# Optimization experiments

Measured on AMD Instinct MI355X. Metric: run time of the kernel, lower is better.

Reference implementation:

```python
import jax, jax.numpy as jnp
from jax import lax
import numpy as np

N, E, L, H, B, R = 12800, 204800, 24, 128, 64, 8
VN, VA = 100, 20


def _p(key, *shape):
    return jax.random.normal(key, shape, dtype=jnp.float32) * 0.05


def setup_inputs() -> dict:
    key = jax.random.key(0)
    ks = jax.random.split(key, 32)
    inp = {
        'nodeTypes': jax.random.randint(ks[0], (N,), 0, VN),
        'edge_index': jax.random.randint(ks[1], (2, E), 0, N),
        'edge_attr': jax.random.randint(ks[2], (E,), 0, R),
        'bs': jnp.repeat(jnp.arange(B, dtype=jnp.int32), N // B),
        'sequence_input': jax.random.uniform(ks[3], (N, L), dtype=jnp.float32),
        'nodes_bs': jnp.full((B,), N // B, dtype=jnp.int32),
        'len_seq': jnp.full((B,), L, dtype=jnp.int32),
        'action_input': jax.random.randint(ks[4], (B,), 0, VA),
        # parameters (RGCN weights SHARED across the 2 layers, as in the source)
        'emb_nodes_w': _p(ks[5], VN, H),
        'emb_actions_w': _p(ks[6], VA, H),
        'rgcn_W': _p(ks[7], R, H, H),
        'rgcn_root': _p(ks[8], H, H),
        'rgcn_b': _p(ks[9], H),
        'gru_Wih': _p(ks[10], 3 * H, H),
        'gru_Whh': _p(ks[11], 3 * H, H),
        'gru_bih': _p(ks[12], 3 * H),
        'gru_bhh': _p(ks[13], 3 * H),
        'linA_w': _p(ks[14], H, H),
        'linA_b': _p(ks[15], H),
        'linAf_w': _p(ks[16], VA, H),
        'linAf_b': _p(ks[17], VA),
        'linN_w': _p(ks[18], H, 2 * H),
        'linN_b': _p(ks[19], H),
        'linNf_w': _p(ks[20], 1, H),
        'linNf_b': _p(ks[21], 1),
        'fin_w': _p(ks[22], H, H),
        'fin_b': _p(ks[23], H),
        'finf_w': _p(ks[24], 1, H),
        'finf_b': _p(ks[25], 1),
    }
    return inp


def _rgcn(x, src, dst, etype, W, Wroot, b):
    # PyG RGCNConv: per-relation mean aggregation, then per-relation weight, plus root + bias
    comb = dst * R + etype  # combined (node, relation) segment id
    msg = jax.ops.segment_sum(x[src], comb, num_segments=N * R)  # [N*R, H]
    cnt = jax.ops.segment_sum(jnp.ones((src.shape[0],), x.dtype), comb, num_segments=N * R)
    mean = (msg / jnp.maximum(cnt, 1.0)[:, None]).reshape(N, R, H)
    return jnp.einsum('nrh,rhd->nd', mean, W) + x @ Wroot + b


def _gru(x_seq, h0, Wih, Whh, bih, bhh):
    # torch GRU gate order: r, z, n ; x_seq [B, T, H]
    def step(h, x):
        gi = x @ Wih.T + bih
        gh = h @ Whh.T + bhh
        i_r, i_z, i_n = jnp.split(gi, 3, axis=-1)
        h_r, h_z, h_n = jnp.split(gh, 3, axis=-1)
        r = jax.nn.sigmoid(i_r + h_r)
        z = jax.nn.sigmoid(i_z + h_z)
        n = jnp.tanh(i_n + r * h_n)
        h_new = (1.0 - z) * n + z * h
        return h_new, h_new
    _, ys = lax.scan(step, h0, jnp.swapaxes(x_seq, 0, 1))
    return jnp.swapaxes(ys, 0, 1)


def _seg_softmax(x, seg, nseg):
    m = jax.ops.segment_max(x, seg, num_segments=nseg)
    e = jnp.exp(x - m[seg])
    s = jax.ops.segment_sum(e, seg, num_segments=nseg)
    return e / s[seg]


def reference(nodeTypes, edge_index, edge_attr, bs, sequence_input, nodes_bs, len_seq,
              action_input, emb_nodes_w, emb_actions_w, rgcn_W, rgcn_root, rgcn_b,
              gru_Wih, gru_Whh, gru_bih, gru_bhh, linA_w, linA_b, linAf_w, linAf_b,
              linN_w, linN_b, linNf_w, linNf_b, fin_w, fin_b, finf_w, finf_b):
    src, dst = edge_index[0], edge_index[1]
    x = emb_nodes_w[nodeTypes]
    for _ in range(2):  # shared-weight RGCN layers + ReLU
        x = jax.nn.relu(_rgcn(x, src, dst, edge_attr, rgcn_W, rgcn_root, rgcn_b))
    nodeEmb = x  # [N, H]

    cnt = jax.ops.segment_sum(jnp.ones((N,), x.dtype), bs, num_segments=B)
    h_G = jax.ops.segment_sum(nodeEmb, bs, num_segments=B) / cnt[:, None]  # [B, H]

    action = jax.nn.relu(h_G @ linA_w.T + linA_b) @ linAf_w.T + linAf_b  # [B, VA]
    final = jax.nn.sigmoid(jax.nn.relu(h_G @ fin_w.T + fin_b) @ finf_w.T + finf_b)  # [B, 1]

    sos = emb_actions_w[action_input][:, None, :]  # [B, 1, H]
    # scatter-sum of per-timestep weighted node embeddings -> [B, L, H]
    emb_seq = sequence_input[:, :, None] * nodeEmb[:, None, :]  # [N, L, H]
    agg = jax.ops.segment_sum(emb_seq, bs, num_segments=B)
    input_gru = jnp.concatenate([sos, agg], axis=1)[:, :L]  # len_seq == L drops last step
    seq = _gru(input_gru, h_G, gru_Wih, gru_Whh, gru_bih, gru_bhh)  # [B, L, H]

    # linNodes(cat(out_gru, nodeEmb)) computed without materializing the [N,L,2H] concat
    part1 = jnp.einsum('blh,oh->blo', seq, linN_w[:, :H])[bs]      # [N, L, H]
    part2 = nodeEmb @ linN_w[:, H:].T                               # [N, H]
    hidden = jax.nn.relu(part1 + part2[:, None, :] + linN_b)       # [N, L, H]
    logits = jnp.einsum('nlh,h->nl', hidden, linNf_w[0]) + linNf_b[0]  # [N, L]
    nodes_final = _seg_softmax(logits, bs, B)
    return (action, nodes_final, final)
```

## Files before the change

kernel.cpp:

```cpp
#include <hip/hip_runtime.h>
#include <math.h>

#define NN 12800
#define NE 204800
#define LL 24
#define HH 128
#define BB 64
#define RR 8
#define VAx 20
#define KC 1152
#define CHK 8
#define PS 16

typedef __attribute__((ext_vector_type(8))) short bf16x8;
typedef __attribute__((ext_vector_type(4))) float f32x4;

__device__ inline unsigned short f2bf(float f) {
  unsigned u = __float_as_uint(f);
  unsigned r = u + 0x7FFF + ((u >> 16) & 1);
  return (unsigned short)(r >> 16);
}
__device__ inline float bf2f(unsigned short s) {
  return __uint_as_float(((unsigned)s) << 16);
}
__device__ inline unsigned packbf(float lo, float hi) {
  return (unsigned)f2bf(lo) | ((unsigned)f2bf(hi) << 16);
}

__global__ void k_prep(const float* __restrict__ rgcnW, const float* __restrict__ rgcnRoot,
                       unsigned short* __restrict__ wcatT,
                       const float* __restrict__ linN_w, unsigned short* __restrict__ linN2bt,
                       const float* __restrict__ Wih, unsigned short* __restrict__ Wihbt,
                       const float* __restrict__ Whh, float* __restrict__ WhhT,
                       const float* __restrict__ linA_w, float* __restrict__ linAT,
                       const float* __restrict__ fin_w, float* __restrict__ finT,
                       unsigned short* __restrict__ linN1bt,
                       const int* __restrict__ nt, const float* __restrict__ embN,
                       unsigned int* __restrict__ x, int* __restrict__ deg) {
  int idx = blockIdx.x * 256 + threadIdx.x;
  if (idx < HH * KC) {
    int d = idx / KC, k = idx - d * KC;
    float v = (k < 1024) ? rgcnW[(k >> 7) * (HH * HH) + (k & 127) * HH + d]
                         : rgcnRoot[(k - 1024) * HH + d];
    wcatT[idx] = f2bf(v);
    return;
  }
  idx -= HH * KC;
  if (idx < HH * HH) {
    int d = idx >> 7, k = idx & 127;
    linN2bt[idx] = f2bf(linN_w[d * 2 * HH + HH + k]);
    return;
  }
  idx -= HH * HH;
  if (idx < 3 * HH * HH) {
    Wihbt[idx] = f2bf(Wih[idx]);
    return;
  }
  idx -= 3 * HH * HH;
  if (idx < 3 * HH * HH) {
    int r = idx / HH, c = idx - r * HH;
    WhhT[c * 384 + r] = Whh[r * HH + c];
    return;
  }
  idx -= 3 * HH * HH;
  if (idx < HH * HH) {
    int r = idx >> 7, c = idx & 127;
    linAT[c * HH + r] = linA_w[r * HH + c];
    return;
  }
  idx -= HH * HH;
  if (idx < HH * HH) {
    int r = idx >> 7, c = idx & 127;
    finT[c * HH + r] = fin_w[r * HH + c];
    return;
  }
  idx -= HH * HH;
  if (idx < HH * HH) {
    int o = idx >> 7, k = idx & 127;
    linN1bt[idx] = f2bf(linN_w[o * 2 * HH + k]);
    return;
  }
  idx -= HH * HH;
  if (idx < NN * 64) {
    int n = idx >> 6, p = idx & 63;
    const float* e = embN + (size_t)nt[n] * HH + p * 2;
    x[idx] = packbf(e[0], e[1]);
    return;
  }
  idx -= NN * 64;
  if (idx < NN * PS) deg[idx] = 0;
}
#define PREP_TOTAL (HH * KC + HH * HH + 3 * HH * HH + 3 * HH * HH + HH * HH + HH * HH + HH * HH + NN * 64 + NN * PS)

__global__ void k_count(const int* __restrict__ edst, int* __restrict__ deg,
                        const int* __restrict__ bs, int* __restrict__ bptr) {
  int i = blockIdx.x * 256 + threadIdx.x;
  if (i < NE) atomicAdd(&deg[edst[i] * PS], 1);
  if (i < NN) {
    int b = bs[i];
    if (i == 0 || bs[i - 1] != b) bptr[b] = i;
    if (i == NN - 1) bptr[BB] = NN;
  }
}

__global__ __launch_bounds__(1024) void k_scane(const int* __restrict__ deg,
                                                int* __restrict__ indptr,
                                                int* __restrict__ cur) {
  __shared__ int ws[16];
  int tid = threadIdx.x;
  const int per = (NN + 1023) >> 10;
  int i0 = tid * per;
  int s = 0;
  for (int k = 0; k < per; ++k) {
    int i = i0 + k;
    if (i < NN) s += deg[i * PS];
  }
  int lane = tid & 63, wv = tid >> 6;
  int incl = s;
#pragma unroll
  for (int off = 1; off < 64; off <<= 1) {
    int t = __shfl_up(incl, off);
    if (lane >= off) incl += t;
  }
  if (lane == 63) ws[wv] = incl;
  __syncthreads();
  if (tid < 16) {
    int v = ws[tid];
    int inc = v;
#pragma unroll
    for (int off = 1; off < 16; off <<= 1) {
      int t = __shfl_up(inc, off);
      if (tid >= off) inc += t;
    }
    ws[tid] = inc - v;
  }
  __syncthreads();
  int run = ws[wv] + incl - s;
  for (int k = 0; k < per; ++k) {
    int i = i0 + k;
    if (i < NN) {
      indptr[i] = run;
      cur[i * PS] = run;
      run += deg[i * PS];
      if (i == NN - 1) indptr[NN] = run;
    }
  }
}

__global__ void k_scattere(const int* __restrict__ esrc, const int* __restrict__ edst,
                           const int* __restrict__ erel, int* __restrict__ cur,
                           int* __restrict__ esort) {
  int i = blockIdx.x * 256 + threadIdx.x;
  if (i >= NE) return;
  int p = atomicAdd(&cur[edst[i] * PS], 1);
  esort[p] = esrc[i] | (erel[i] << 16);
}

__global__ __launch_bounds__(256) void k_agg(const unsigned int* __restrict__ x,
                                             const int* __restrict__ indptr,
                                             const int* __restrict__ esort,
                                             unsigned int* __restrict__ A, int n0, int nc) {
  int wid = ((blockIdx.x * 256) + threadIdx.x) >> 6;
  int lane = threadIdx.x & 63;
  if (wid >= nc) return;
  int n = n0 + wid;
  float a0=0,a1=0,a2=0,a3=0,a4=0,a5=0,a6=0,a7=0;
  float b0=0,b1=0,b2=0,b3=0,b4=0,b5=0,b6=0,b7=0;
  int c0=0,c1=0,c2=0,c3=0,c4=0,c5=0,c6=0,c7=0;
  int e0 = indptr[n], e1 = indptr[n + 1];

#define ACCV(RV, VV)                                                              \
  {                                                                               \
    float v0_ = bf2f((unsigned short)((VV) & 0xFFFF));                            \
    float v1_ = bf2f((unsigned short)((VV) >> 16));                               \
    switch (RV) {                                                                 \
      case 0: a0 += v0_; b0 += v1_; c0++; break;                                  \
      case 1: a1 += v0_; b1 += v1_; c1++; break;                                  \
      case 2: a2 += v0_; b2 += v1_; c2++; break;                                  \
      case 3: a3 += v0_; b3 += v1_; c3++; break;                                  \
      case 4: a4 += v0_; b4 += v1_; c4++; break;                                  \
      case 5: a5 += v0_; b5 += v1_; c5++; break;                                  \
      case 6: a6 += v0_; b6 += v1_; c6++; break;                                  \
      default: a7 += v0_; b7 += v1_; c7++; break;                                 \
    }                                                                             \
  }

  int e = e0;
  for (; e + 4 <= e1; e += 4) {
    int pk0 = esort[e], pk1 = esort[e + 1], pk2 = esort[e + 2], pk3 = esort[e + 3];
    unsigned v0 = x[(size_t)(pk0 & 0xFFFF) * 64 + lane];
    unsigned v1 = x[(size_t)(pk1 & 0xFFFF) * 64 + lane];
    unsigned v2 = x[(size_t)(pk2 & 0xFFFF) * 64 + lane];
    unsigned v3 = x[(size_t)(pk3 & 0xFFFF) * 64 + lane];
    ACCV(pk0 >> 16, v0);
    ACCV(pk1 >> 16, v1);
    ACCV(pk2 >> 16, v2);
    ACCV(pk3 >> 16, v3);
  }
  for (; e < e1; ++e) {
    int pk = esort[e];
    unsigned v = x[(size_t)(pk & 0xFFFF) * 64 + lane];
    ACCV(pk >> 16, v);
  }
#undef ACCV

  unsigned int* Ar = A + (size_t)wid * (KC / 2);
  float i0 = 1.0f / (float)(c0 > 0 ? c0 : 1);
  float i1 = 1.0f / (float)(c1 > 0 ? c1 : 1);
  float i2 = 1.0f / (float)(c2 > 0 ? c2 : 1);
  float i3 = 1.0f / (float)(c3 > 0 ? c3 : 1);
  float i4 = 1.0f / (float)(c4 > 0 ? c4 : 1);
  float i5 = 1.0f / (float)(c5 > 0 ? c5 : 1);
  float i6 = 1.0f / (float)(c6 > 0 ? c6 : 1);
  float i7 = 1.0f / (float)(c7 > 0 ? c7 : 1);
  Ar[0 * 64 + lane] = packbf(a0 * i0, b0 * i0);
  Ar[1 * 64 + lane] = packbf(a1 * i1, b1 * i1);
  Ar[2 * 64 + lane] = packbf(a2 * i2, b2 * i2);
  Ar[3 * 64 + lane] = packbf(a3 * i3, b3 * i3);
  Ar[4 * 64 + lane] = packbf(a4 * i4, b4 * i4);
  Ar[5 * 64 + lane] = packbf(a5 * i5, b5 * i5);
  Ar[6 * 64 + lane] = packbf(a6 * i6, b6 * i6);
  Ar[7 * 64 + lane] = packbf(a7 * i7, b7 * i7);
  Ar[512 + lane] = x[n * 64 + lane];
}

template <int OUTMODE>
__global__ __launch_bounds__(256) void k_mgemm(const unsigned short* __restrict__ Abf, int lda,
                                               const unsigned short* __restrict__ BTbf, int ldb,
                                               const float* __restrict__ bias,
                                               void* __restrict__ C, int ldc, int M, int K) {
  __shared__ unsigned int ldsu[(8192 + 16384) / 4];
  char* ldsc = (char*)ldsu;
  int tid = threadIdx.x;
  int m0 = blockIdx.x * 64;
  int n0c = blockIdx.y * 128;
  int w = tid >> 6, l = tid & 63;
  int lrow = l & 15, lg = l >> 4;
  f32x4 acc[8] = {};

  const char* Ab = (const char*)Abf;
  const char* Bb = (const char*)(BTbf + (size_t)n0c * ldb);
  int KT = K >> 6;
  for (int kt = 0; kt < KT; ++kt) {
    int k0 = kt << 6;
#pragma unroll
    for (int i = 0; i < 2; ++i) {
      int slot = i * 256 + tid;
      int row = slot >> 3;
      int colb = (slot & 7) << 4;
      int gr = m0 + row;
      gr = gr < M ? gr : M - 1;
      size_t srcb = ((size_t)gr * lda + k0) * 2 + (size_t)(colb ^ ((row & 7) << 4));
      __builtin_amdgcn_global_load_lds((const unsigned int*)(Ab + srcb),
                                       (unsigned int*)(ldsc + slot * 16), 16, 0, 0);
    }
#pragma unroll
    for (int i = 0; i < 4; ++i) {
      int slot = i * 256 + tid;
      int row = slot >> 3;
      int colb = (slot & 7) << 4;
      size_t srcb = ((size_t)row * ldb + k0) * 2 + (size_t)(colb ^ ((row & 7) << 4));
      __builtin_amdgcn_global_load_lds((const unsigned int*)(Bb + srcb),
                                       (unsigned int*)(ldsc + 8192 + slot * 16), 16, 0, 0);
    }
    __syncthreads();
#pragma unroll
    for (int h = 0; h < 2; ++h) {
      int arow = w * 16 + lrow;
      bf16x8 af = *(const bf16x8*)(ldsc + arow * 128 +
                                   ((h * 64 + lg * 16) ^ ((arow & 7) << 4)));
#pragma unroll
      for (int c = 0; c < 8; ++c) {
        int brow = c * 16 + lrow;
        bf16x8 bf = *(const bf16x8*)(ldsc + 8192 + brow * 128 +
                                     ((h * 64 + lg * 16) ^ ((brow & 7) << 4)));
        acc[c] = __builtin_amdgcn_mfma_f32_16x16x32_bf16(af, bf, acc[c], 0, 0, 0);
      }
    }
    __syncthreads();
  }
#pragma unroll
  for (int c = 0; c < 8; ++c) {
#pragma unroll
    for (int r = 0; r < 4; ++r) {
      int gm = m0 + w * 16 + lg * 4 + r;
      if (gm >= M) continue;
      int gn = n0c + c * 16 + lrow;
      float v = acc[c][r];
      if (OUTMODE == 1) {
        v = fmaxf(v + bias[gn], 0.f);
        ((unsigned short*)C)[(size_t)gm * ldc + gn] = f2bf(v);
      } else if (OUTMODE == 2) {
        ((float*)C)[(size_t)gm * ldc + gn] = v + bias[gn];
      } else {
        ((float*)C)[(size_t)gm * ldc + gn] = v;
      }
    }
  }
}

__global__ __launch_bounds__(256) void k_aggS_part(const float* __restrict__ seqin,
                                                   const unsigned short* __restrict__ x,
                                                   const int* __restrict__ bptr,
                                                   float* __restrict__ part) {
  int bc = blockIdx.x, b = bc >> 3, c = bc & 7;
  int h = threadIdx.x & 127, l0 = threadIdx.x >> 7;
  int i0 = bptr[b], i1 = bptr[b + 1];
  int len = i1 - i0;
  int per = (len + CHK - 1) / CHK;
  int j0 = i0 + c * per;
  int j1 = j0 + per;
  if (j1 > i1) j1 = i1;
  float acc[12] = {};
  float esum = 0.f;
  for (int n = j0; n < j1; ++n) {
    float e = bf2f(x[n * HH + h]);
    esum += e;
    const float* srow = seqin + (size_t)n * LL;
#pragma unroll
    for (int t = 0; t < 12; ++t) acc[t] = fmaf(srow[l0 + 2 * t], e, acc[t]);
  }
  float* p = part + (size_t)bc * 25 * HH + h;
#pragma unroll
  for (int t = 0; t < 12; ++t) p[(l0 + 2 * t) * HH] = acc[t];
  if (l0 == 0) p[24 * HH] = esum;
}

__global__ void k_aggS_red(const float* __restrict__ part, const int* __restrict__ bptr,
                           const float* __restrict__ embA, const int* __restrict__ act,
                           unsigned short* __restrict__ ig, float* __restrict__ hG) {
  int idx = blockIdx.x * 256 + threadIdx.x;
  if (idx >= BB * 25 * HH) return;
  int h = idx & 127;
  int rem = idx >> 7;
  int l = rem % 25, b = rem / 25;
  if (l == 23) {
    ig[((size_t)b * LL) * HH + h] = f2bf(embA[(size_t)act[b] * HH + h]);
    return;
  }
  float s = 0.f;
#pragma unroll
  for (int c = 0; c < CHK; ++c) s += part[(((size_t)(b * CHK + c)) * 25 + l) * HH + h];
  if (l == 24) {
    int len = bptr[b + 1] - bptr[b];
    hG[b * HH + h] = s / (float)len;
  } else {
    ig[((size_t)b * LL + l + 1) * HH + h] = f2bf(s);
  }
}

__global__ __launch_bounds__(128) void k_heads(const float* __restrict__ hG,
                                               const float* __restrict__ linAT,
                                               const float* __restrict__ linA_b,
                                               const float* __restrict__ linAf_w,
                                               const float* __restrict__ linAf_b,
                                               const float* __restrict__ finT,
                                               const float* __restrict__ fin_b,
                                               const float* __restrict__ finf_w,
                                               const float* __restrict__ finf_b,
                                               float* __restrict__ outA,
                                               float* __restrict__ outF) {
  int b = blockIdx.x >> 1, which = blockIdx.x & 1, j = threadIdx.x;
  __shared__ float hsh[HH], t1[HH];
  hsh[j] = hG[b * HH + j];
  __syncthreads();
  const float* Wt = which ? finT : linAT;
  const float* bb = which ? fin_b : linA_b;
  float s = bb[j];
  for (int k = 0; k < HH; ++k) s = fmaf(hsh[k], Wt[k * HH + j], s);
  t1[j] = fmaxf(s, 0.f);
  __syncthreads();
  if (which == 0) {
    if (j < VAx) {
      float o = linAf_b[j];
      for (int k = 0; k < HH; ++k) o = fmaf(t1[k], linAf_w[j * HH + k], o);
      outA[b * VAx + j] = o;
    }
  } else if (j == 0) {
    float o = finf_b[0];
    for (int k = 0; k < HH; ++k) o = fmaf(t1[k], finf_w[k], o);
    outF[b] = 1.f / (1.f + expf(-o));
  }
}

__global__ __launch_bounds__(384) void k_gru(const float* __restrict__ gi,
                                             const float* __restrict__ WhhT,
                                             const float* __restrict__ bhh,
                                             const float* __restrict__ hG,
                                             unsigned short* __restrict__ seqout) {
  int b = blockIdx.x, tid = threadIdx.x;
  int gate = tid >> 7, j = tid & 127;
  __shared__ float h[HH];
  __shared__ float sz[HH], sg[HH];
  float w[HH];
#pragma unroll
  for (int k = 0; k < HH; ++k) w[k] = WhhT[k * 384 + tid];
  float bh = bhh[tid];
  if (tid < HH) h[tid] = hG[b * HH + tid];
  __syncthreads();
  const float* gib = gi + (size_t)b * LL * 384;
  for (int t = 0; t < LL; ++t) {
    float giv = gib[t * 384 + tid];
    float gin = (gate == 0) ? gib[t * 384 + 256 + j] : 0.f;
    float hj = h[j];
    float g0 = 0.f, g1 = 0.f, g2 = 0.f, g3 = 0.f;
    const float4* h4 = (const float4*)h;
#pragma unroll
    for (int k4 = 0; k4 < HH / 4; ++k4) {
      float4 hv = h4[k4];
      g0 = fmaf(w[4 * k4 + 0], hv.x, g0);
      g1 = fmaf(w[4 * k4 + 1], hv.y, g1);
      g2 = fmaf(w[4 * k4 + 2], hv.z, g2);
      g3 = fmaf(w[4 * k4 + 3], hv.w, g3);
    }
    float g = bh + ((g0 + g1) + (g2 + g3));
    float r = 0.f;
    if (gate == 0) {
      r = 1.f / (1.f + expf(-(giv + g)));
    } else if (gate == 1) {
      sz[j] = 1.f / (1.f + expf(-(giv + g)));
    } else {
      sg[j] = g;
    }
    __syncthreads();
    if (gate == 0) {
      float n = tanhf(gin + r * sg[j]);
      float z = sz[j];
      float hn = (1.f - z) * n + z * hj;
      h[j] = hn;
      seqout[((size_t)b * LL + t) * HH + j] = f2bf(hn);
    }
    __syncthreads();
  }
}

__global__ __launch_bounds__(256) void k_logits(const float* __restrict__ part1,
                                                const float* __restrict__ part2,
                                                const float* __restrict__ linN_b,
                                                const float* __restrict__ linNf_w,
                                                const float* __restrict__ linNf_b,
                                                const int* __restrict__ bs,
                                                float* __restrict__ logits) {
  int wid = ((blockIdx.x * 256) + threadIdx.x) >> 6;
  int lane = threadIdx.x & 63;
  if (wid >= NN) return;
  int n = wid;
  int b = bs[n];
  float p2a = part2[n * HH + lane] + linN_b[lane];
  float p2b = part2[n * HH + 64 + lane] + linN_b[64 + lane];
  float wa = linNf_w[lane], wb = linNf_w[64 + lane];
  const float* p1 = part1 + (size_t)b * LL * HH;
  float bf = linNf_b[0];
  for (int l = 0; l < LL; ++l) {
    float v = fmaxf(p1[l * HH + lane] + p2a, 0.f) * wa +
              fmaxf(p1[l * HH + 64 + lane] + p2b, 0.f) * wb;
#pragma unroll
    for (int off = 32; off > 0; off >>= 1) v += __shfl_down(v, off);
    if (lane == 0) logits[n * LL + l] = v + bf;
  }
}

__global__ __launch_bounds__(64) void k_softmax(const float* __restrict__ logits,
                                                const int* __restrict__ bptr,
                                                float* __restrict__ outN) {
  int b = blockIdx.x / LL, l = blockIdx.x % LL;
  int lane = threadIdx.x;
  int i0 = bptr[b], i1 = bptr[b + 1];
  float m = -1e30f;
  for (int i = i0 + lane; i < i1; i += 64) m = fmaxf(m, logits[i * LL + l]);
#pragma unroll
  for (int off = 32; off > 0; off >>= 1) m = fmaxf(m, __shfl_xor(m, off));
  float s = 0.f;
  for (int i = i0 + lane; i < i1; i += 64) s += expf(logits[i * LL + l] - m);
#pragma unroll
  for (int off = 32; off > 0; off >>= 1) s += __shfl_xor(s, off);
  float inv = 1.f / s;
  for (int i = i0 + lane; i < i1; i += 64) {
    outN[i * LL + l] = expf(logits[i * LL + l] - m) * inv;
  }
}

extern "C" void kernel_launch(void* const* d_in, const int* in_sizes, int n_in,
                              void* d_out, int out_size, void* d_ws, size_t ws_size,
                              hipStream_t stream) {
  const int* nodeTypes = (const int*)d_in[0];
  const int* esrc = (const int*)d_in[1];
  const int* edst = esrc + NE;
  const int* erel = (const int*)d_in[2];
  const int* bs = (const int*)d_in[3];
  const float* seqin = (const float*)d_in[4];
  const int* actin = (const int*)d_in[7];
  const float* embN = (const float*)d_in[8];
  const float* embA = (const float*)d_in[9];
  const float* rgcnW = (const float*)d_in[10];
  const float* rgcnRoot = (const float*)d_in[11];
  const float* rgcnB = (const float*)d_in[12];
  const float* Wih = (const float*)d_in[13];
  const float* Whh = (const float*)d_in[14];
  const float* bih = (const float*)d_in[15];
  const float* bhh = (const float*)d_in[16];
  const float* linA_w = (const float*)d_in[17];
  const float* linA_b = (const float*)d_in[18];
  const float* linAf_w = (const float*)d_in[19];
  const float* linAf_b = (const float*)d_in[20];
  const float* linN_w = (const float*)d_in[21];
  const float* linN_b = (const float*)d_in[22];
  const float* linNf_w = (const float*)d_in[23];
  const float* linNf_b = (const float*)d_in[24];
  const float* fin_w = (const float*)d_in[25];
  const float* fin_b = (const float*)d_in[26];
  const float* finf_w = (const float*)d_in[27];
  const float* finf_b = (const float*)d_in[28];

  float* outA = (float*)d_out;
  float* outNodes = outA + BB * VAx;
  float* outF = outNodes + (size_t)NN * LL;

  char* basep = (char*)d_ws;
  size_t off = 0;
  auto alloc = [&](size_t bytes) -> void* {
    void* p = basep + off;
    off = (off + bytes + 255) & ~(size_t)255;
    return p;
  };

  unsigned int* x = (unsigned int*)alloc(sizeof(unsigned int) * NN * 64);
  unsigned int* x2 = (unsigned int*)alloc(sizeof(unsigned int) * NN * 64);
  float* hG = (float*)alloc(sizeof(float) * BB * HH);
  unsigned short* wcatT = (unsigned short*)alloc(sizeof(unsigned short) * HH * KC);
  unsigned short* linN2bt = (unsigned short*)alloc(sizeof(unsigned short) * HH * HH);
  unsigned short* Wihbt = (unsigned short*)alloc(sizeof(unsigned short) * 3 * HH * HH);
  unsigned short* linN1bt = (unsigned short*)alloc(sizeof(unsigned short) * HH * HH);
  float* WhhT = (float*)alloc(sizeof(float) * HH * 3 * HH);
  float* linAT = (float*)alloc(sizeof(float) * HH * HH);
  float* finT = (float*)alloc(sizeof(float) * HH * HH);
  float* part = (float*)alloc(sizeof(float) * BB * CHK * 25 * HH);
  unsigned short* ig = (unsigned short*)alloc(sizeof(unsigned short) * BB * LL * HH);
  float* gi = (float*)alloc(sizeof(float) * BB * LL * 3 * HH);
  unsigned short* seqb = (unsigned short*)alloc(sizeof(unsigned short) * BB * LL * HH);
  float* part1 = (float*)alloc(sizeof(float) * BB * LL * HH);
  float* part2 = (float*)alloc(sizeof(float) * NN * HH);
  float* logitsB = (float*)alloc(sizeof(float) * NN * LL);
  int* deg = (int*)alloc(sizeof(int) * NN * PS);
  int* cur = (int*)alloc(sizeof(int) * NN * PS);
  int* indptr = (int*)alloc(sizeof(int) * (NN + 1));
  int* esort = (int*)alloc(sizeof(int) * NE);
  int* bptr = (int*)alloc(sizeof(int) * (BB + 1));

  size_t remain = (ws_size > off) ? (ws_size - off) : 0;
  int NCk = NN;
  while ((size_t)NCk * KC * 2 > remain && NCk > 100) NCk >>= 1;
  unsigned int* A = (unsigned int*)alloc((size_t)NCk * (KC / 2) * sizeof(unsigned int));

  k_prep<<<(PREP_TOTAL + 255) / 256, 256, 0, stream>>>(
      rgcnW, rgcnRoot, wcatT, linN_w, linN2bt, Wih, Wihbt, Whh, WhhT, linA_w, linAT,
      fin_w, finT, linN1bt, nodeTypes, embN, x, deg);

  k_count<<<(NE + 255) / 256, 256, 0, stream>>>(edst, deg, bs, bptr);
  k_scane<<<1, 1024, 0, stream>>>(deg, indptr, cur);
  k_scattere<<<(NE + 255) / 256, 256, 0, stream>>>(esrc, edst, erel, cur, esort);

  const unsigned int* xin = x;
  unsigned int* xout = x2;
  for (int layer = 0; layer < 2; ++layer) {
    for (int n0 = 0; n0 < NN; n0 += NCk) {
      int nc = NN - n0 < NCk ? NN - n0 : NCk;
      k_agg<<<(nc + 3) / 4, 256, 0, stream>>>(xin, indptr, esort, A, n0, nc);
      dim3 g((nc + 63) / 64, 1);
      k_mgemm<1><<<g, 256, 0, stream>>>(
          (const unsigned short*)A, KC, wcatT, KC, rgcnB,
          (void*)((unsigned short*)xout + (size_t)n0 * HH), HH, nc, KC);
    }
    const unsigned int* t = xin;
    xin = xout;
    xout = (unsigned int*)t;
  }
  const unsigned short* nodeEmb = (const unsigned short*)xin;

  k_aggS_part<<<BB * CHK, 256, 0, stream>>>(seqin, nodeEmb, bptr, part);
  k_aggS_red<<<(BB * 25 * HH + 255) / 256, 256, 0, stream>>>(part, bptr, embA, actin, ig, hG);

  k_heads<<<2 * BB, HH, 0, stream>>>(hG, linAT, linA_b, linAf_w, linAf_b, finT, fin_b,
                                     finf_w, finf_b, outA, outF);

  {
    dim3 g((BB * LL) / 64, 3);
    k_mgemm<2><<<g, 256, 0, stream>>>(ig, HH, Wihbt, HH, bih, (void*)gi, 3 * HH,
                                      BB * LL, HH);
  }
  k_gru<<<BB, 384, 0, stream>>>(gi, WhhT, bhh, hG, seqb);

  {
    dim3 g((BB * LL) / 64, 1);
    k_mgemm<0><<<g, 256, 0, stream>>>(seqb, HH, linN1bt, HH, nullptr, (void*)part1, HH,
                                      BB * LL, HH);
  }
  {
    dim3 g(NN / 64, 1);
    k_mgemm<0><<<g, 256, 0, stream>>>(nodeEmb, HH, linN2bt, HH, nullptr, (void*)part2, HH,
                                      NN, HH);
  }
  k_logits<<<NN / 4, 256, 0, stream>>>(part1, part2, linN_b, linNf_w, linNf_b, bs, logitsB);
  k_softmax<<<BB * LL, 64, 0, stream>>>(logitsB, bptr, outNodes);
}
```

Baseline: 265.0 us.

## Fuse RGCN aggregation with GEMM via LDS and merge small kernels

The per-layer aggregation and the RGCN GEMM are fused into one kernel. Each 512-thread block aggregates 64 node rows into 147KB of swizzled LDS, then runs MFMA against the weights read straight from global memory. This removes the round trip of the large bf16 A matrix through HBM and two launches per layer. The small GEMMs become single-shot specializations, the heads are folded into the GRU launch, and the two linNodes GEMMs share one launch. The risks are very low occupancy (one block per CU because of the LDS size) and uncached B-operand loads from global memory inside the K loop.

```diff
diff --git a/kernel.cpp b/kernel.cpp
--- a/kernel.cpp
+++ b/kernel.cpp
@@ -11,6 +11,7 @@
 #define KC 1152
 #define CHK 8
 #define PS 16
+#define RGCN_LDS (64 * KC * 2)
 
 typedef __attribute__((ext_vector_type(8))) short bf16x8;
 typedef __attribute__((ext_vector_type(4))) float f32x4;
@@ -156,79 +157,116 @@
   esort[p] = esrc[i] | (erel[i] << 16);
 }
 
-__global__ __launch_bounds__(256) void k_agg(const unsigned int* __restrict__ x,
-                                             const int* __restrict__ indptr,
-                                             const int* __restrict__ esort,
-                                             unsigned int* __restrict__ A, int n0, int nc) {
-  int wid = ((blockIdx.x * 256) + threadIdx.x) >> 6;
-  int lane = threadIdx.x & 63;
-  if (wid >= nc) return;
-  int n = n0 + wid;
-  float a0=0,a1=0,a2=0,a3=0,a4=0,a5=0,a6=0,a7=0;
-  float b0=0,b1=0,b2=0,b3=0,b4=0,b5=0,b6=0,b7=0;
-  int c0=0,c1=0,c2=0,c3=0,c4=0,c5=0,c6=0,c7=0;
-  int e0 = indptr[n], e1 = indptr[n + 1];
-
+__global__ __launch_bounds__(512) void k_rgcn(const unsigned int* __restrict__ x,
+                                              const int* __restrict__ indptr,
+                                              const int* __restrict__ esort,
+                                              const unsigned short* __restrict__ BT,
+                                              const float* __restrict__ bias,
+                                              unsigned short* __restrict__ xout) {
+  extern __shared__ char lds[];
+  int tid = threadIdx.x;
+  int w = tid >> 6, lane = tid & 63;
+  int m0 = blockIdx.x * 64;
+
+  for (int i = 0; i < 8; ++i) {
+    int row = w * 8 + i;
+    int n = m0 + row;
+    float a0=0,a1=0,a2=0,a3=0,a4=0,a5=0,a6=0,a7=0;
+    float b0=0,b1=0,b2=0,b3=0,b4=0,b5=0,b6=0,b7=0;
+    int c0=0,c1=0,c2=0,c3=0,c4=0,c5=0,c6=0,c7=0;
+    int e0 = indptr[n], e1 = indptr[n + 1];
 #define ACCV(RV, VV)                                                              \
-  {                                                                               \
-    float v0_ = bf2f((unsigned short)((VV) & 0xFFFF));                            \
-    float v1_ = bf2f((unsigned short)((VV) >> 16));                               \
-    switch (RV) {                                                                 \
-      case 0: a0 += v0_; b0 += v1_; c0++; break;                                  \
-      case 1: a1 += v0_; b1 += v1_; c1++; break;                                  \
-      case 2: a2 += v0_; b2 += v1_; c2++; break;                                  \
-      case 3: a3 += v0_; b3 += v1_; c3++; break;                                  \
-      case 4: a4 += v0_; b4 += v1_; c4++; break;                                  \
-      case 5: a5 += v0_; b5 += v1_; c5++; break;                                  \
-      case 6: a6 += v0_; b6 += v1_; c6++; break;                                  \
-      default: a7 += v0_; b7 += v1_; c7++; break;                                 \
-    }                                                                             \
-  }
-
-  int e = e0;
-  for (; e + 4 <= e1; e += 4) {
-    int pk0 = esort[e], pk1 = esort[e + 1], pk2 = esort[e + 2], pk3 = esort[e + 3];
-    unsigned v0 = x[(size_t)(pk0 & 0xFFFF) * 64 + lane];
-    unsigned v1 = x[(size_t)(pk1 & 0xFFFF) * 64 + lane];
-    unsigned v2 = x[(size_t)(pk2 & 0xFFFF) * 64 + lane];
-    unsigned v3 = x[(size_t)(pk3 & 0xFFFF) * 64 + lane];
-    ACCV(pk0 >> 16, v0);
-    ACCV(pk1 >> 16, v1);
-    ACCV(pk2 >> 16, v2);
-    ACCV(pk3 >> 16, v3);
-  }
-  for (; e < e1; ++e) {
-    int pk = esort[e];
-    unsigned v = x[(size_t)(pk & 0xFFFF) * 64 + lane];
-    ACCV(pk >> 16, v);
-  }
+    {                                                                             \
+      float v0_ = bf2f((unsigned short)((VV) & 0xFFFF));                          \
+      float v1_ = bf2f((unsigned short)((VV) >> 16));                             \
+      switch (RV) {                                                               \
+        case 0: a0 += v0_; b0 += v1_; c0++; break;                                \
+        case 1: a1 += v0_; b1 += v1_; c1++; break;                                \
+        case 2: a2 += v0_; b2 += v1_; c2++; break;                                \
+        case 3: a3 += v0_; b3 += v1_; c3++; break;                                \
+        case 4: a4 += v0_; b4 += v1_; c4++; break;                                \
+        case 5: a5 += v0_; b5 += v1_; c5++; break;                                \
+        case 6: a6 += v0_; b6 += v1_; c6++; break;                                \
+        default: a7 += v0_; b7 += v1_; c7++; break;                               \
+      }                                                                           \
+    }
+    int e = e0;
+    for (; e + 4 <= e1; e += 4) {
+      int pk0 = esort[e], pk1 = esort[e + 1], pk2 = esort[e + 2], pk3 = esort[e + 3];
+      unsigned v0 = x[(size_t)(pk0 & 0xFFFF) * 64 + lane];
+      unsigned v1 = x[(size_t)(pk1 & 0xFFFF) * 64 + lane];
+      unsigned v2 = x[(size_t)(pk2 & 0xFFFF) * 64 + lane];
+      unsigned v3 = x[(size_t)(pk3 & 0xFFFF) * 64 + lane];
+      ACCV(pk0 >> 16, v0);
+      ACCV(pk1 >> 16, v1);
+      ACCV(pk2 >> 16, v2);
+      ACCV(pk3 >> 16, v3);
+    }
+    for (; e < e1; ++e) {
+      int pk = esort[e];
+      unsigned v = x[(size_t)(pk & 0xFFFF) * 64 + lane];
+      ACCV(pk >> 16, v);
+    }
 #undef ACCV
-
-  unsigned int* Ar = A + (size_t)wid * (KC / 2);
-  float i0 = 1.0f / (float)(c0 > 0 ? c0 : 1);
-  float i1 = 1.0f / (float)(c1 > 0 ? c1 : 1);
-  float i2 = 1.0f / (float)(c2 > 0 ? c2 : 1);
-  float i3 = 1.0f / (float)(c3 > 0 ? c3 : 1);
-  float i4 = 1.0f / (float)(c4 > 0 ? c4 : 1);
-  float i5 = 1.0f / (float)(c5 > 0 ? c5 : 1);
-  float i6 = 1.0f / (float)(c6 > 0 ? c6 : 1);
-  float i7 = 1.0f / (float)(c7 > 0 ? c7 : 1);
-  Ar[0 * 64 + lane] = packbf(a0 * i0, b0 * i0);
-  Ar[1 * 64 + lane] = packbf(a1 * i1, b1 * i1);
-  Ar[2 * 64 + lane] = packbf(a2 * i2, b2 * i2);
-  Ar[3 * 64 + lane] = packbf(a3 * i3, b3 * i3);
-  Ar[4 * 64 + lane] = packbf(a4 * i4, b4 * i4);
-  Ar[5 * 64 + lane] = packbf(a5 * i5, b5 * i5);
-  Ar[6 * 64 + lane] = packbf(a6 * i6, b6 * i6);
-  Ar[7 * 64 + lane] = packbf(a7 * i7, b7 * i7);
-  Ar[512 + lane] = x[n * 64 + lane];
-}
-
-template <int OUTMODE>
-__global__ __launch_bounds__(256) void k_mgemm(const unsigned short* __restrict__ Abf, int lda,
-                                               const unsigned short* __restrict__ BTbf, int ldb,
-                                               const float* __restrict__ bias,
-                                               void* __restrict__ C, int ldc, int M, int K) {
+    char* Ar = lds + row * (KC * 2);
+    int sw = (row & 7) << 4;
+    float i0v = 1.0f / (float)(c0 > 0 ? c0 : 1);
+    float i1v = 1.0f / (float)(c1 > 0 ? c1 : 1);
+    float i2v = 1.0f / (float)(c2 > 0 ? c2 : 1);
+    float i3v = 1.0f / (float)(c3 > 0 ? c3 : 1);
+    float i4v = 1.0f / (float)(c4 > 0 ? c4 : 1);
+    float i5v = 1.0f / (float)(c5 > 0 ? c5 : 1);
+    float i6v = 1.0f / (float)(c6 > 0 ? c6 : 1);
+    float i7v = 1.0f / (float)(c7 > 0 ? c7 : 1);
+    *(unsigned*)(Ar + ((0 * 256 + lane * 4) ^ sw)) = packbf(a0 * i0v, b0 * i0v);
+    *(unsigned*)(Ar + ((1 * 256 + lane * 4) ^ sw)) = packbf(a1 * i1v, b1 * i1v);
+    *(unsigned*)(Ar + ((2 * 256 + lane * 4) ^ sw)) = packbf(a2 * i2v, b2 * i2v);
+    *(unsigned*)(Ar + ((3 * 256 + lane * 4) ^ sw)) = packbf(a3 * i3v, b3 * i3v);
+    *(unsigned*)(Ar + ((4 * 256 + lane * 4) ^ sw)) = packbf(a4 * i4v, b4 * i4v);
+    *(unsigned*)(Ar + ((5 * 256 + lane * 4) ^ sw)) = packbf(a5 * i5v, b5 * i5v);
+    *(unsigned*)(Ar + ((6 * 256 + lane * 4) ^ sw)) = packbf(a6 * i6v, b6 * i6v);
+    *(unsigned*)(Ar + ((7 * 256 + lane * 4) ^ sw)) = packbf(a7 * i7v, b7 * i7v);
+    *(unsigned*)(Ar + ((2048 + lane * 4) ^ sw)) = x[(size_t)n * 64 + lane];
+  }
+  __syncthreads();
+
+  int lrow = lane & 15, lg = lane >> 4;
+  int wrow = w & 3, wcol = w >> 2;
+  f32x4 acc[4] = {};
+  int arow = wrow * 16 + lrow;
+  const char* Abase = lds + arow * (KC * 2);
+  int asw = (arow & 7) << 4;
+  const char* Bb = (const char*)BT;
+#pragma unroll 3
+  for (int kt = 0; kt < KC / 64; ++kt) {
+#pragma unroll
+    for (int h = 0; h < 2; ++h) {
+      bf16x8 af = *(const bf16x8*)(Abase + ((kt * 128 + h * 64 + lg * 16) ^ asw));
+#pragma unroll
+      for (int c = 0; c < 4; ++c) {
+        int brow = (wcol * 4 + c) * 16 + lrow;
+        bf16x8 bfr = *(const bf16x8*)(Bb + (size_t)brow * (KC * 2) + kt * 128 + h * 64 + lg * 16);
+        acc[c] = __builtin_amdgcn_mfma_f32_16x16x32_bf16(af, bfr, acc[c], 0, 0, 0);
+      }
+    }
+  }
+#pragma unroll
+  for (int c = 0; c < 4; ++c) {
+    int gn = (wcol * 4 + c) * 16 + lrow;
+    float bv = bias[gn];
+#pragma unroll
+    for (int r = 0; r < 4; ++r) {
+      int gm = m0 + wrow * 16 + lg * 4 + r;
+      float v = fmaxf(acc[c][r] + bv, 0.f);
+      xout[(size_t)gm * HH + gn] = f2bf(v);
+    }
+  }
+}
+
+__global__ __launch_bounds__(256) void k_mgemm_gi(const unsigned short* __restrict__ Abf,
+                                                  const unsigned short* __restrict__ BTbf,
+                                                  const float* __restrict__ bias,
+                                                  float* __restrict__ C, int M) {
   __shared__ unsigned int ldsu[(8192 + 16384) / 4];
   char* ldsc = (char*)ldsu;
   int tid = threadIdx.x;
@@ -237,64 +275,116 @@
   int w = tid >> 6, l = tid & 63;
   int lrow = l & 15, lg = l >> 4;
   f32x4 acc[8] = {};
-
   const char* Ab = (const char*)Abf;
-  const char* Bb = (const char*)(BTbf + (size_t)n0c * ldb);
-  int KT = K >> 6;
-  for (int kt = 0; kt < KT; ++kt) {
-    int k0 = kt << 6;
+  const char* Bb = (const char*)(BTbf + (size_t)n0c * HH);
+  {
 #pragma unroll
     for (int i = 0; i < 2; ++i) {
       int slot = i * 256 + tid;
-      int row = slot >> 3;
-      int colb = (slot & 7) << 4;
-      int gr = m0 + row;
-      gr = gr < M ? gr : M - 1;
-      size_t srcb = ((size_t)gr * lda + k0) * 2 + (size_t)(colb ^ ((row & 7) << 4));
+      int row = slot >> 4;
+      int colb = (slot & 15) << 4;
+      size_t srcb = ((size_t)(m0 + row) * HH) * 2 + (size_t)(colb ^ ((row & 7) << 4));
       __builtin_amdgcn_global_load_lds((const unsigned int*)(Ab + srcb),
                                        (unsigned int*)(ldsc + slot * 16), 16, 0, 0);
     }
 #pragma unroll
     for (int i = 0; i < 4; ++i) {
       int slot = i * 256 + tid;
-      int row = slot >> 3;
-      int colb = (slot & 7) << 4;
-      size_t srcb = ((size_t)row * ldb + k0) * 2 + (size_t)(colb ^ ((row & 7) << 4));
+      int row = slot >> 4;
+      int colb = (slot & 15) << 4;
+      size_t srcb = ((size_t)row * HH) * 2 + (size_t)(colb ^ ((row & 7) << 4));
       __builtin_amdgcn_global_load_lds((const unsigned int*)(Bb + srcb),
-                                       (unsigned int*)(ldsc + 8192 + slot * 16), 16, 0, 0);
+                                       (unsigned int*)(ldsc + 16384 + slot * 16), 16, 0, 0);
     }
     __syncthreads();
 #pragma unroll
-    for (int h = 0; h < 2; ++h) {
+    for (int h = 0; h < 4; ++h) {
       int arow = w * 16 + lrow;
-      bf16x8 af = *(const bf16x8*)(ldsc + arow * 128 +
-                                   ((h * 64 + lg * 16) ^ ((arow & 7) << 4)));
+      bf16x8 af = *(const bf16x8*)(ldsc + arow * 256 + ((h * 64 + lg * 16) ^ ((arow & 7) << 4)));
 #pragma unroll
       for (int c = 0; c < 8; ++c) {
         int brow = c * 16 + lrow;
-        bf16x8 bf = *(const bf16x8*)(ldsc + 8192 + brow * 128 +
-                                     ((h * 64 + lg * 16) ^ ((brow & 7) << 4)));
-        acc[c] = __builtin_amdgcn_mfma_f32_16x16x32_bf16(af, bf, acc[c], 0, 0, 0);
+        bf16x8 bfr = *(const bf16x8*)(ldsc + 16384 + brow * 256 +
+                                      ((h * 64 + lg * 16) ^ ((brow & 7) << 4)));
+        acc[c] = __builtin_amdgcn_mfma_f32_16x16x32_bf16(af, bfr, acc[c], 0, 0, 0);
       }
     }
-    __syncthreads();
   }
 #pragma unroll
   for (int c = 0; c < 8; ++c) {
 #pragma unroll
     for (int r = 0; r < 4; ++r) {
       int gm = m0 + w * 16 + lg * 4 + r;
-      if (gm >= M) continue;
       int gn = n0c + c * 16 + lrow;
-      float v = acc[c][r];
-      if (OUTMODE == 1) {
-        v = fmaxf(v + bias[gn], 0.f);
-        ((unsigned short*)C)[(size_t)gm * ldc + gn] = f2bf(v);
-      } else if (OUTMODE == 2) {
-        ((float*)C)[(size_t)gm * ldc + gn] = v + bias[gn];
-      } else {
-        ((float*)C)[(size_t)gm * ldc + gn] = v;
+      C[(size_t)gm * (3 * HH) + gn] = acc[c][r] + bias[gn];
+    }
+  }
+}
+
+__global__ __launch_bounds__(256) void k_mgemm_dual(const unsigned short* __restrict__ A2,
+                                                    const unsigned short* __restrict__ BT2,
+                                                    float* __restrict__ C2,
+                                                    const unsigned short* __restrict__ A1,
+                                                    const unsigned short* __restrict__ BT1,
+                                                    float* __restrict__ C1) {
+  __shared__ unsigned int ldsu[(8192 + 16384) / 4];
+  char* ldsc = (char*)ldsu;
+  int tid = threadIdx.x;
+  int bid = blockIdx.x;
+  const unsigned short* Abf;
+  const unsigned short* BTbf;
+  float* C;
+  int m0;
+  if (bid < NN / 64) {
+    Abf = A2; BTbf = BT2; C = C2; m0 = bid * 64;
+  } else {
+    Abf = A1; BTbf = BT1; C = C1; m0 = (bid - NN / 64) * 64;
+  }
+  int w = tid >> 6, l = tid & 63;
+  int lrow = l & 15, lg = l >> 4;
+  f32x4 acc[8] = {};
+  const char* Ab = (const char*)Abf;
+  const char* Bb = (const char*)BTbf;
+  {
+#pragma unroll
+    for (int i = 0; i < 2; ++i) {
+      int slot = i * 256 + tid;
+      int row = slot >> 4;
+      int colb = (slot & 15) << 4;
+      size_t srcb = ((size_t)(m0 + row) * HH) * 2 + (size_t)(colb ^ ((row & 7) << 4));
+      __builtin_amdgcn_global_load_lds((const unsigned int*)(Ab + srcb),
+                                       (unsigned int*)(ldsc + slot * 16), 16, 0, 0);
+    }
+#pragma unroll
+    for (int i = 0; i < 4; ++i) {
+      int slot = i * 256 + tid;
+      int row = slot >> 4;
+      int colb = (slot & 15) << 4;
+      size_t srcb = ((size_t)row * HH) * 2 + (size_t)(colb ^ ((row & 7) << 4));
+      __builtin_amdgcn_global_load_lds((const unsigned int*)(Bb + srcb),
+                                       (unsigned int*)(ldsc + 16384 + slot * 16), 16, 0, 0);
+    }
+    __syncthreads();
+#pragma unroll
+    for (int h = 0; h < 4; ++h) {
+      int arow = w * 16 + lrow;
+      bf16x8 af = *(const bf16x8*)(ldsc + arow * 256 + ((h * 64 + lg * 16) ^ ((arow & 7) << 4)));
+#pragma unroll
+      for (int c = 0; c < 8; ++c) {
+        int brow = c * 16 + lrow;
+        bf16x8 bfr = *(const bf16x8*)(ldsc + 16384 + brow * 256 +
+                                      ((h * 64 + lg * 16) ^ ((brow & 7) << 4)));
+        acc[c] = __builtin_amdgcn_mfma_f32_16x16x32_bf16(af, bfr, acc[c], 0, 0, 0);
       }
+    }
+  }
+#pragma unroll
+  for (int c = 0; c < 8; ++c) {
+#pragma unroll
+    for (int r = 0; r < 4; ++r) {
+      int gm = m0 + w * 16 + lg * 4 + r;
+      int gn = c * 16 + lrow;
+      C[(size_t)gm * HH + gn] = acc[c][r];
     }
   }
 }
@@ -349,46 +439,50 @@
   }
 }
 
-__global__ __launch_bounds__(128) void k_heads(const float* __restrict__ hG,
-                                               const float* __restrict__ linAT,
-                                               const float* __restrict__ linA_b,
-                                               const float* __restrict__ linAf_w,
-                                               const float* __restrict__ linAf_b,
-                                               const float* __restrict__ finT,
-                                               const float* __restrict__ fin_b,
-                                               const float* __restrict__ finf_w,
-                                               const float* __restrict__ finf_b,
-                                               float* __restrict__ outA,
-                                               float* __restrict__ outF) {
-  int b = blockIdx.x >> 1, which = blockIdx.x & 1, j = threadIdx.x;
-  __shared__ float hsh[HH], t1[HH];
-  hsh[j] = hG[b * HH + j];
-  __syncthreads();
-  const float* Wt = which ? finT : linAT;
-  const float* bb = which ? fin_b : linA_b;
-  float s = bb[j];
-  for (int k = 0; k < HH; ++k) s = fmaf(hsh[k], Wt[k * HH + j], s);
-  t1[j] = fmaxf(s, 0.f);
-  __syncthreads();
-  if (which == 0) {
-    if (j < VAx) {
-      float o = linAf_b[j];
-      for (int k = 0; k < HH; ++k) o = fmaf(t1[k], linAf_w[j * HH + k], o);
-      outA[b * VAx + j] = o;
-    }
-  } else if (j == 0) {
-    float o = finf_b[0];
-    for (int k = 0; k < HH; ++k) o = fmaf(t1[k], finf_w[k], o);
-    outF[b] = 1.f / (1.f + expf(-o));
-  }
-}
-
-__global__ __launch_bounds__(384) void k_gru(const float* __restrict__ gi,
-                                             const float* __restrict__ WhhT,
-                                             const float* __restrict__ bhh,
-                                             const float* __restrict__ hG,
-                                             unsigned short* __restrict__ seqout) {
-  int b = blockIdx.x, tid = threadIdx.x;
+__global__ __launch_bounds__(384) void k_gruheads(const float* __restrict__ gi,
+                                                  const float* __restrict__ WhhT,
+                                                  const float* __restrict__ bhh,
+                                                  const float* __restrict__ hG,
+                                                  unsigned short* __restrict__ seqout,
+                                                  const float* __restrict__ linAT,
+                                                  const float* __restrict__ linA_b,
+                                                  const float* __restrict__ linAf_w,
+                                                  const float* __restrict__ linAf_b,
+                                                  const float* __restrict__ finT,
+                                                  const float* __restrict__ fin_b,
+                                                  const float* __restrict__ finf_w,
+                                                  const float* __restrict__ finf_b,
+                                                  float* __restrict__ outA,
+                                                  float* __restrict__ outF) {
+  int tid = threadIdx.x;
+  if (blockIdx.x >= BB) {
+    int hb = blockIdx.x - BB;
+    int b = hb >> 1, which = hb & 1, j = tid;
+    __shared__ float hsh[HH], t1[HH];
+    if (j < HH) hsh[j] = hG[b * HH + j];
+    __syncthreads();
+    if (j < HH) {
+      const float* Wt = which ? finT : linAT;
+      const float* bb = which ? fin_b : linA_b;
+      float s = bb[j];
+      for (int k = 0; k < HH; ++k) s = fmaf(hsh[k], Wt[k * HH + j], s);
+      t1[j] = fmaxf(s, 0.f);
+    }
+    __syncthreads();
+    if (which == 0) {
+      if (j < VAx) {
+        float o = linAf_b[j];
+        for (int k = 0; k < HH; ++k) o = fmaf(t1[k], linAf_w[j * HH + k], o);
+        outA[b * VAx + j] = o;
+      }
+    } else if (j == 0) {
+      float o = finf_b[0];
+      for (int k = 0; k < HH; ++k) o = fmaf(t1[k], finf_w[k], o);
+      outF[b] = 1.f / (1.f + expf(-o));
+    }
+    return;
+  }
+  int b = blockIdx.x;
   int gate = tid >> 7, j = tid & 127;
   __shared__ float h[HH];
   __shared__ float sz[HH], sg[HH];
@@ -516,6 +610,9 @@
   float* outNodes = outA + BB * VAx;
   float* outF = outNodes + (size_t)NN * LL;
 
+  hipFuncSetAttribute((const void*)k_rgcn, hipFuncAttributeMaxDynamicSharedMemorySize,
+                      RGCN_LDS);
+
   char* basep = (char*)d_ws;
   size_t off = 0;
   auto alloc = [&](size_t bytes) -> void* {
@@ -547,11 +644,6 @@
   int* esort = (int*)alloc(sizeof(int) * NE);
   int* bptr = (int*)alloc(sizeof(int) * (BB + 1));
 
-  size_t remain = (ws_size > off) ? (ws_size - off) : 0;
-  int NCk = NN;
-  while ((size_t)NCk * KC * 2 > remain && NCk > 100) NCk >>= 1;
-  unsigned int* A = (unsigned int*)alloc((size_t)NCk * (KC / 2) * sizeof(unsigned int));
-
   k_prep<<<(PREP_TOTAL + 255) / 256, 256, 0, stream>>>(
       rgcnW, rgcnRoot, wcatT, linN_w, linN2bt, Wih, Wihbt, Whh, WhhT, linA_w, linAT,
       fin_w, finT, linN1bt, nodeTypes, embN, x, deg);
@@ -560,46 +652,25 @@
   k_scane<<<1, 1024, 0, stream>>>(deg, indptr, cur);
   k_scattere<<<(NE + 255) / 256, 256, 0, stream>>>(esrc, edst, erel, cur, esort);
 
-  const unsigned int* xin = x;
-  unsigned int* xout = x2;
-  for (int layer = 0; layer < 2; ++layer) {
-    for (int n0 = 0; n0 < NN; n0 += NCk) {
-      int nc = NN - n0 < NCk ? NN - n0 : NCk;
-      k_agg<<<(nc + 3) / 4, 256, 0, stream>>>(xin, indptr, esort, A, n0, nc);
-      dim3 g((nc + 63) / 64, 1);
-      k_mgemm<1><<<g, 256, 0, stream>>>(
-          (const unsigned short*)A, KC, wcatT, KC, rgcnB,
-          (void*)((unsigned short*)xout + (size_t)n0 * HH), HH, nc, KC);
-    }
-    const unsigned int* t = xin;
-    xin = xout;
-    xout = (unsigned int*)t;
-  }
-  const unsigned short* nodeEmb = (const unsigned short*)xin;
+  k_rgcn<<<NN / 64, 512, RGCN_LDS, stream>>>(x, indptr, esort, wcatT, rgcnB,
+                                             (unsigned short*)x2);
+  k_rgcn<<<NN / 64, 512, RGCN_LDS, stream>>>(x2, indptr, esort, wcatT, rgcnB,
+                                             (unsigned short*)x);
+  const unsigned short* nodeEmb = (const unsigned short*)x;
 
   k_aggS_part<<<BB * CHK, 256, 0, stream>>>(seqin, nodeEmb, bptr, part);
   k_aggS_red<<<(BB * 25 * HH + 255) / 256, 256, 0, stream>>>(part, bptr, embA, actin, ig, hG);
 
-  k_heads<<<2 * BB, HH, 0, stream>>>(hG, linAT, linA_b, linAf_w, linAf_b, finT, fin_b,
-                                     finf_w, finf_b, outA, outF);
-
   {
     dim3 g((BB * LL) / 64, 3);
-    k_mgemm<2><<<g, 256, 0, stream>>>(ig, HH, Wihbt, HH, bih, (void*)gi, 3 * HH,
-                                      BB * LL, HH);
-  }
-  k_gru<<<BB, 384, 0, stream>>>(gi, WhhT, bhh, hG, seqb);
-
-  {
-    dim3 g((BB * LL) / 64, 1);
-    k_mgemm<0><<<g, 256, 0, stream>>>(seqb, HH, linN1bt, HH, nullptr, (void*)part1, HH,
-                                      BB * LL, HH);
-  }
-  {
-    dim3 g(NN / 64, 1);
-    k_mgemm<0><<<g, 256, 0, stream>>>(nodeEmb, HH, linN2bt, HH, nullptr, (void*)part2, HH,
-                                      NN, HH);
-  }
+    k_mgemm_gi<<<g, 256, 0, stream>>>(ig, Wihbt, bih, gi, BB * LL);
+  }
+  k_gruheads<<<BB + 2 * BB, 384, 0, stream>>>(gi, WhhT, bhh, hG, seqb, linAT, linA_b,
+                                              linAf_w, linAf_b, finT, fin_b, finf_w,
+                                              finf_b, outA, outF);
+
+  k_mgemm_dual<<<NN / 64 + (BB * LL) / 64, 256, 0, stream>>>(nodeEmb, linN2bt, part2,
+                                                             seqb, linN1bt, part1);
   k_logits<<<NN / 4, 256, 0, stream>>>(part1, part2, linN_b, linNf_w, linNf_b, bs, logitsB);
   k_softmax<<<BB * LL, 64, 0, stream>>>(logitsB, bptr, outNodes);
 }
```

New measurement: 325.0 us. +22.7%, slower.
